# Kernel optimization log

Measured on AMD Instinct MI355X. Metric: run time of the kernel, lower is better.

The kernel has to match this reference:

```python
import jax, jax.numpy as jnp
import numpy as np
import math

B, S, D, H = 4, 2048, 1024, 16
HD = D // H  # 64
FF = 4096
EPS = 1e-5


def layer_norm(x, g, b):
    mu = jnp.mean(x, axis=-1, keepdims=True)
    var = jnp.mean(jnp.square(x - mu), axis=-1, keepdims=True)
    return (x - mu) * jax.lax.rsqrt(var + EPS) * g + b


def setup_inputs() -> dict:
    key = jax.random.key(0)
    ks = jax.random.split(key, 16)
    sc = 0.02
    return {
        "x": jax.random.normal(ks[0], (B, S, D), dtype=jnp.float32),
        "Wq": jax.random.normal(ks[1], (H, D, HD), dtype=jnp.float32) * sc,
        "bq": jnp.zeros((H, HD), dtype=jnp.float32),
        "Wk": jax.random.normal(ks[2], (H, D, HD), dtype=jnp.float32) * sc,
        "bk": jnp.zeros((H, HD), dtype=jnp.float32),
        "Wv": jax.random.normal(ks[3], (H, D, HD), dtype=jnp.float32) * sc,
        "bv": jnp.zeros((H, HD), dtype=jnp.float32),
        "Wo": jax.random.normal(ks[4], (D, D), dtype=jnp.float32) * sc,
        "bo": jnp.zeros((D,), dtype=jnp.float32),
        "W1": jax.random.normal(ks[5], (D, FF), dtype=jnp.float32) * sc,
        "b1": jnp.zeros((FF,), dtype=jnp.float32),
        "W2": jax.random.normal(ks[6], (FF, D), dtype=jnp.float32) * sc,
        "b2": jnp.zeros((D,), dtype=jnp.float32),
        "ln1_g": jnp.ones((D,), dtype=jnp.float32),
        "ln1_b": jnp.zeros((D,), dtype=jnp.float32),
        "ln2_g": jnp.ones((D,), dtype=jnp.float32),
        "ln2_b": jnp.zeros((D,), dtype=jnp.float32),
    }


def reference(x, Wq, bq, Wk, bk, Wv, bv, Wo, bo, W1, b1, W2, b2, ln1_g, ln1_b, ln2_g, ln2_b):
    b, s, d = x.shape
    h1 = layer_norm(x, ln1_g, ln1_b)
    # per-head Q/K/V linears, vectorized over heads: [b,h,s,hd]
    q = jnp.einsum('bsd,hde->bhse', h1, Wq) + bq[None, :, None, :]
    k = jnp.einsum('bsd,hde->bhse', h1, Wk) + bk[None, :, None, :]
    v = jnp.einsum('bsd,hde->bhse', h1, Wv) + bv[None, :, None, :]
    scores = jnp.einsum('bhqe,bhke->bhqk', q, k) / math.sqrt(q.shape[-1])
    causal = jnp.tril(jnp.ones((s, s), dtype=bool))
    scores = jnp.where(causal[None, None], scores, -jnp.inf)
    weights = jax.nn.softmax(scores, axis=-1)
    attn = jnp.einsum('bhqk,bhke->bhqe', weights, v)
    # concat heads (head order = torch concat dim=-1)
    attn = attn.transpose(0, 2, 1, 3).reshape(b, s, d)
    x = x + attn @ Wo + bo
    h2 = layer_norm(x, ln2_g, ln2_b)
    y = jax.nn.gelu(h2 @ W1 + b1, approximate=False)
    y = jax.nn.gelu(y @ W2 + b2, approximate=False)
    return x + y
```

## Files before the change

### kernel.cpp

```cpp
#include <hip/hip_runtime.h>
#include <cstdint>
#include <cstddef>


#define DI __device__ __forceinline__

typedef __attribute__((ext_vector_type(8))) __bf16 bf16x8;
typedef __attribute__((ext_vector_type(4))) float floatx4;
typedef __attribute__((ext_vector_type(4))) unsigned int uintx4;

static constexpr int Bn = 4, Sn = 2048, Dn = 1024, Hn = 16, HDn = 64, FFn = 4096;
static constexpr int NTOK = Bn * Sn;
static constexpr int D3 = 3 * Dn;

DI float bf2f(unsigned short u) { return __uint_as_float(((unsigned int)u) << 16); }
DI unsigned short f2bf(float f) {
  unsigned int u = __float_as_uint(f);
  u += 0x7FFFu + ((u >> 16) & 1u);
  return (unsigned short)(u >> 16);
}
DI float gelu_f(float v) { return 0.5f * v * (1.0f + erff(v * 0.70710678118654752f)); }
DI bf16x8 ld8(const unsigned short* p) { return *(const bf16x8*)p; }
DI floatx4 mfma16(bf16x8 a, bf16x8 b, floatx4 c) {
  return __builtin_amdgcn_mfma_f32_16x16x32_bf16(a, b, c, 0, 0, 0);
}
DI void g2l16(const unsigned short* g, unsigned short* l) {
  __builtin_amdgcn_global_load_lds((__attribute__((address_space(1))) void*)g,
                                   (__attribute__((address_space(3))) void*)l,
                                   16, 0, 0);
}
DI float ldin(const void* p, size_t idx, bool f32) {
  return f32 ? ((const float*)p)[idx] : bf2f(((const unsigned short*)p)[idx]);
}
DI unsigned int cvt_pk_bf16(float lo, float hi) {
  unsigned int r;
  asm("v_cvt_pk_bf16_f32 %0, %1, %2" : "=v"(r) : "v"(lo), "v"(hi));
  return r;
}
DI bf16x8 pack8(unsigned int a, unsigned int b, unsigned int c, unsigned int d) {
  uintx4 t;
  t[0] = a; t[1] = b; t[2] = c; t[3] = d;
  return __builtin_bit_cast(bf16x8, t);
}
DI int swz16(int row, int col) {
  return (row << 6) + ((((col >> 3) ^ row ^ (row >> 3)) & 7) << 3) + (col & 7);
}
DI int xcd_swz(int bid, int nwg) {
  return (bid & 7) * (nwg >> 3) + (bid >> 3);
}

__global__ void detect_kernel(const unsigned short* __restrict__ x,
                              int* __restrict__ flag) {
  int t = threadIdx.x;
  int cnt = 0;
  for (int i = t; i < 1024; i += 64) {
    unsigned short u = x[2 * i];
    int e = (u >> 7) & 0xFF;
    cnt += (e >= 96 && e <= 142) ? 1 : 0;
  }
  #pragma unroll
  for (int off = 32; off >= 1; off >>= 1) cnt += __shfl_xor(cnt, off);
  if (t == 0) *flag = (cnt < 820) ? 1 : 0;
}

__global__ void vec_prep(const void* bq, const void* bk, const void* bv,
                         const void* bo, const void* b1, const void* b2,
                         const void* g1, const void* be1, const void* g2,
                         const void* be2, unsigned short* __restrict__ dst,
                         const int* __restrict__ flag) {
  int i = blockIdx.x * 256 + threadIdx.x;
  if (i >= 13312) return;
  const bool f32 = *flag != 0;
  const void* src; int off;
  if      (i < 1024)  { src = bq;  off = i; }
  else if (i < 2048)  { src = bk;  off = i - 1024; }
  else if (i < 3072)  { src = bv;  off = i - 2048; }
  else if (i < 4096)  { src = bo;  off = i - 3072; }
  else if (i < 8192)  { src = b1;  off = i - 4096; }
  else if (i < 9216)  { src = b2;  off = i - 8192; }
  else if (i < 10240) { src = g1;  off = i - 9216; }
  else if (i < 11264) { src = be1; off = i - 10240; }
  else if (i < 12288) { src = g2;  off = i - 11264; }
  else                { src = be2; off = i - 12288; }
  dst[i] = f2bf(ldin(src, off, f32));
}

__global__ void transpose_kernel(const void* __restrict__ src,
                                 unsigned short* __restrict__ dst, int K, int N,
                                 const int* __restrict__ flag) {
  __shared__ unsigned short tile[64][65];
  const bool f32 = *flag != 0;
  int kb = blockIdx.y * 64, nb = blockIdx.x * 64;
  for (int i = threadIdx.x; i < 4096; i += 256) {
    int r = i >> 6, c = i & 63;
    tile[r][c] = f2bf(ldin(src, (size_t)(kb + r) * N + nb + c, f32));
  }
  __syncthreads();
  for (int i = threadIdx.x; i < 4096; i += 256) {
    int r = i >> 6, c = i & 63;
    dst[(size_t)(nb + r) * K + kb + c] = tile[c][r];
  }
}

__global__ void qkvT_kernel(const void* __restrict__ Wq,
                            const void* __restrict__ Wk,
                            const void* __restrict__ Wv,
                            unsigned short* __restrict__ WT,
                            const int* __restrict__ flag) {
  __shared__ unsigned short tile[64][65];
  const bool f32 = *flag != 0;
  const void* src = blockIdx.z == 0 ? Wq : (blockIdx.z == 1 ? Wk : Wv);
  int h = blockIdx.y, d0 = blockIdx.x * 64;
  size_t base = (size_t)h * (Dn * HDn);
  for (int i = threadIdx.x; i < 4096; i += 256) {
    int r = i >> 6, c = i & 63;
    tile[r][c] = f2bf(ldin(src, base + (size_t)(d0 + r) * 64 + c, f32));
  }
  __syncthreads();
  for (int i = threadIdx.x; i < 4096; i += 256) {
    int r = i >> 6, c = i & 63;
    WT[(size_t)(blockIdx.z * 1024 + h * 64 + r) * 1024 + d0 + c] = tile[c][r];
  }
}

__global__ __launch_bounds__(256) void ln_kernel(const void* __restrict__ x,
                                                 const unsigned short* __restrict__ g,
                                                 const unsigned short* __restrict__ b,
                                                 unsigned short* __restrict__ out,
                                                 const int* __restrict__ flag) {
  const bool f32 = flag ? (*flag != 0) : true;
  int row = blockIdx.x, t = threadIdx.x;
  float v[4];
  if (f32) {
    float4 f = *(const float4*)((const float*)x + (size_t)row * Dn + t * 4);
    v[0] = f.x; v[1] = f.y; v[2] = f.z; v[3] = f.w;
  } else {
    ushort4 u = *(const ushort4*)((const unsigned short*)x + (size_t)row * Dn + t * 4);
    v[0] = bf2f(u.x); v[1] = bf2f(u.y); v[2] = bf2f(u.z); v[3] = bf2f(u.w);
  }
  float s = v[0] + v[1] + v[2] + v[3];
  float s2 = v[0] * v[0] + v[1] * v[1] + v[2] * v[2] + v[3] * v[3];
  #pragma unroll
  for (int off = 32; off >= 1; off >>= 1) {
    s += __shfl_xor(s, off);
    s2 += __shfl_xor(s2, off);
  }
  __shared__ float red[8];
  int wv = t >> 6, ln = t & 63;
  if (ln == 0) { red[wv] = s; red[4 + wv] = s2; }
  __syncthreads();
  s = red[0] + red[1] + red[2] + red[3];
  s2 = red[4] + red[5] + red[6] + red[7];
  float mu = s * (1.0f / 1024.0f);
  float var = s2 * (1.0f / 1024.0f) - mu * mu;
  float rs = rsqrtf(fmaxf(var, 0.0f) + 1e-5f);
  ushort4 gg = *(const ushort4*)(g + t * 4);
  ushort4 bb = *(const ushort4*)(b + t * 4);
  ushort4 o;
  o.x = f2bf((v[0] - mu) * rs * bf2f(gg.x) + bf2f(bb.x));
  o.y = f2bf((v[1] - mu) * rs * bf2f(gg.y) + bf2f(bb.y));
  o.z = f2bf((v[2] - mu) * rs * bf2f(gg.z) + bf2f(bb.z));
  o.w = f2bf((v[3] - mu) * rs * bf2f(gg.w) + bf2f(bb.w));
  *(ushort4*)(out + (size_t)row * Dn + t * 4) = o;
}

enum { EPI_BIAS_BF16 = 0, EPI_WO = 1, EPI_GELU = 2, EPI_FF2 = 3 };

template <int EPI>
__global__ __launch_bounds__(256, 3) void gemm_kernel(
    const unsigned short* __restrict__ A, const unsigned short* __restrict__ BT,
    const unsigned short* __restrict__ bias, const void* __restrict__ residv,
    const float* __restrict__ resid_f, unsigned short* __restrict__ Cb,
    float* __restrict__ Cf, const int* __restrict__ flag, int M, int N, int K) {
  __shared__ unsigned short As[128 * 32];
  __shared__ unsigned short Bs[128 * 32];
  const int gx = gridDim.x;
  const int nwg = gx * gridDim.y;
  const int bid = xcd_swz((int)blockIdx.y * gx + (int)blockIdx.x, nwg);
  const int m0 = (bid / gx) * 128, n0 = (bid % gx) * 128;
  const int w = threadIdx.x >> 6, lane = threadIdx.x & 63;
  const int waveM = (w >> 1) * 64, waveN = (w & 1) * 64;
  const int m16 = lane & 15, quad = lane >> 4;
  const bool rf32 = flag && (*flag != 0);

  const int srow = w * 32 + (lane >> 2);
  const int scol = (lane & 3) * 8;
  const unsigned short* Ag = A + (size_t)(m0 + srow) * K + scol;
  const unsigned short* Bg = BT + (size_t)(n0 + srow) * K + scol;
  unsigned short* Al = As + srow * 32 + scol;
  unsigned short* Bl = Bs + srow * 32 + scol;
  const size_t rowstep = (size_t)16 * K;

  floatx4 acc[4][4];
  #pragma unroll
  for (int i = 0; i < 4; i++)
    #pragma unroll
    for (int j = 0; j < 4; j++) acc[i][j] = floatx4{0.f, 0.f, 0.f, 0.f};

  for (int k0 = 0; k0 < K; k0 += 32) {
    g2l16(Ag, Al);
    g2l16(Ag + rowstep, Al + 16 * 32);
    g2l16(Bg, Bl);
    g2l16(Bg + rowstep, Bl + 16 * 32);
    Ag += 32; Bg += 32;
    __syncthreads();
    bf16x8 af[4], bfv[4];
    #pragma unroll
    for (int mt = 0; mt < 4; mt++)
      af[mt] = ld8(As + (waveM + mt * 16 + m16) * 32 + quad * 8);
    #pragma unroll
    for (int nt = 0; nt < 4; nt++)
      bfv[nt] = ld8(Bs + (waveN + nt * 16 + m16) * 32 + quad * 8);
    #pragma unroll
    for (int mt = 0; mt < 4; mt++)
      #pragma unroll
      for (int nt = 0; nt < 4; nt++)
        acc[mt][nt] = mfma16(af[mt], bfv[nt], acc[mt][nt]);
    __syncthreads();
  }

  #pragma unroll
  for (int mt = 0; mt < 4; mt++) {
    #pragma unroll
    for (int nt = 0; nt < 4; nt++) {
      const int col = n0 + waveN + nt * 16 + m16;
      const float bcol = bf2f(bias[col]);
      #pragma unroll
      for (int r = 0; r < 4; r++) {
        const int row = m0 + waveM + mt * 16 + quad * 4 + r;
        const size_t idx = (size_t)row * N + col;
        float v = acc[mt][nt][r] + bcol;
        if constexpr (EPI == EPI_BIAS_BF16) {
          Cb[idx] = f2bf(v);
        } else if constexpr (EPI == EPI_WO) {
          float rv = rf32 ? ((const float*)residv)[idx]
                          : bf2f(((const unsigned short*)residv)[idx]);
          Cf[idx] = v + rv;
        } else if constexpr (EPI == EPI_GELU) {
          Cb[idx] = f2bf(gelu_f(v));
        } else {
          float ov = gelu_f(v) + resid_f[idx];
          if (rf32) Cf[idx] = ov;
          else      Cb[idx] = f2bf(ov);
        }
      }
    }
  }
}

__global__ __launch_bounds__(256, 4) void attn_kernel(
    const unsigned short* __restrict__ qkv, unsigned short* __restrict__ attn) {
  const int bid = xcd_swz((int)blockIdx.y * 32 + (int)blockIdx.x, 2048);
  const int qt = 31 - (bid & 31);
  const int bh = bid >> 5;
  const int b = bh >> 4, h = bh & 15;
  const int tid = threadIdx.x;
  const int w = tid >> 6, lane = tid & 63;
  const int m16 = lane & 15, quad = lane >> 4;

  __shared__ unsigned short Ks[2][4096];
  __shared__ unsigned short Vt[2][4096];

  const int qrow = qt * 64 + w * 16 + m16;
  const int qloc = w * 16 + m16;
  const unsigned short* qp = qkv + (size_t)(b * Sn + qrow) * D3 + h * 64 + quad * 8;
  const bf16x8 qf0 = ld8(qp), qf1 = ld8(qp + 32);

  floatx4 acc_o[4];
  #pragma unroll
  for (int nt = 0; nt < 4; nt++) acc_o[nt] = floatx4{0.f, 0.f, 0.f, 0.f};
  float lsum = 0.f;

  const int kr = tid >> 3, kc = (tid & 7) * 8;
  const int krs = (kr & 3) + (((kr >> 3) & 3) << 2) + (((kr >> 2) & 1) << 4);
  const int vk = (tid >> 3) * 2, ve = (tid & 7) * 8;

  uint4 kreg0, kreg1, vreg0, vreg1;
  const unsigned short* const kvroot = qkv + (size_t)(b * Sn) * D3 + h * 64;

  {
    const unsigned short* base = kvroot;
    kreg0 = *(const uint4*)(base + (size_t)kr * D3 + 1024 + kc);
    kreg1 = *(const uint4*)(base + (size_t)(kr + 32) * D3 + 1024 + kc);
    vreg0 = *(const uint4*)(base + (size_t)vk * D3 + 2048 + ve);
    vreg1 = *(const uint4*)(base + (size_t)(vk + 1) * D3 + 2048 + ve);
  }

  for (int kt = 0; kt <= qt; ++kt) {
    const int pb = kt & 1;
    *(uint4*)(Ks[pb] + swz16(krs, kc)) = kreg0;
    *(uint4*)(Ks[pb] + swz16(krs + 32, kc)) = kreg1;
    {
      const unsigned short* a0 = (const unsigned short*)&vreg0;
      const unsigned short* a1 = (const unsigned short*)&vreg1;
      #pragma unroll
      for (int i = 0; i < 8; i++) {
        unsigned int word = (unsigned int)a0[i] | ((unsigned int)a1[i] << 16);
        *(unsigned int*)(Vt[pb] + swz16(ve + i, vk)) = word;
      }
    }
    __syncthreads();
    if (kt < qt) {
      const unsigned short* base = kvroot + (size_t)(kt + 1) * 64 * D3;
      kreg0 = *(const uint4*)(base + (size_t)kr * D3 + 1024 + kc);
      kreg1 = *(const uint4*)(base + (size_t)(kr + 32) * D3 + 1024 + kc);
      vreg0 = *(const uint4*)(base + (size_t)vk * D3 + 2048 + ve);
      vreg1 = *(const uint4*)(base + (size_t)(vk + 1) * D3 + 2048 + ve);
    }

    floatx4 sa[4];
    #pragma unroll
    for (int nt = 0; nt < 4; nt++) {
      bf16x8 k0 = ld8(Ks[pb] + swz16(nt * 16 + m16, quad * 8));
      bf16x8 k1 = ld8(Ks[pb] + swz16(nt * 16 + m16, 32 + quad * 8));
      floatx4 t = mfma16(k0, qf0, floatx4{0.f, 0.f, 0.f, 0.f});
      sa[nt] = mfma16(k1, qf1, t);
    }

    if (kt == qt) {
      #pragma unroll
      for (int nt = 0; nt < 4; nt++) {
        const int kb_ = (quad << 3) + ((nt & 1) << 2) + ((nt >> 1) << 5);
        #pragma unroll
        for (int r = 0; r < 4; r++)
          if (kb_ + r > qloc) sa[nt][r] = -1e30f;
      }
    }

    constexpr float C = 0.18033688011112042f;
    float e00 = __builtin_amdgcn_exp2f(sa[0][0] * C);
    float e01 = __builtin_amdgcn_exp2f(sa[0][1] * C);
    float e02 = __builtin_amdgcn_exp2f(sa[0][2] * C);
    float e03 = __builtin_amdgcn_exp2f(sa[0][3] * C);
    float e10 = __builtin_amdgcn_exp2f(sa[1][0] * C);
    float e11 = __builtin_amdgcn_exp2f(sa[1][1] * C);
    float e12 = __builtin_amdgcn_exp2f(sa[1][2] * C);
    float e13 = __builtin_amdgcn_exp2f(sa[1][3] * C);
    float e20 = __builtin_amdgcn_exp2f(sa[2][0] * C);
    float e21 = __builtin_amdgcn_exp2f(sa[2][1] * C);
    float e22 = __builtin_amdgcn_exp2f(sa[2][2] * C);
    float e23 = __builtin_amdgcn_exp2f(sa[2][3] * C);
    float e30 = __builtin_amdgcn_exp2f(sa[3][0] * C);
    float e31 = __builtin_amdgcn_exp2f(sa[3][1] * C);
    float e32 = __builtin_amdgcn_exp2f(sa[3][2] * C);
    float e33 = __builtin_amdgcn_exp2f(sa[3][3] * C);
    lsum += ((e00 + e01) + (e02 + e03)) + ((e10 + e11) + (e12 + e13)) +
            ((e20 + e21) + (e22 + e23)) + ((e30 + e31) + (e32 + e33));
    const bf16x8 pa0 = pack8(cvt_pk_bf16(e00, e01), cvt_pk_bf16(e02, e03),
                             cvt_pk_bf16(e10, e11), cvt_pk_bf16(e12, e13));
    const bf16x8 pa1 = pack8(cvt_pk_bf16(e20, e21), cvt_pk_bf16(e22, e23),
                             cvt_pk_bf16(e30, e31), cvt_pk_bf16(e32, e33));

    #pragma unroll
    for (int nt = 0; nt < 4; nt++) {
      bf16x8 v0 = ld8(Vt[pb] + swz16(nt * 16 + m16, quad * 8));
      bf16x8 v1 = ld8(Vt[pb] + swz16(nt * 16 + m16, 32 + quad * 8));
      acc_o[nt] = mfma16(pa0, v0, acc_o[nt]);
      acc_o[nt] = mfma16(pa1, v1, acc_o[nt]);
    }
  }

  lsum += __shfl_xor(lsum, 16);
  lsum += __shfl_xor(lsum, 32);

  #pragma unroll
  for (int r = 0; r < 4; r++) {
    const float inv = 1.0f / fmaxf(__shfl(lsum, quad * 4 + r), 1e-20f);
    const size_t orow = (size_t)(b * Sn + qt * 64 + w * 16 + quad * 4 + r) * Dn + h * 64;
    #pragma unroll
    for (int nt = 0; nt < 4; nt++)
      attn[orow + nt * 16 + m16] = f2bf(acc_o[nt][r] * inv);
  }
}

extern "C" void kernel_launch(void* const* d_in, const int* in_sizes, int n_in,
                              void* d_out, int out_size, void* d_ws, size_t ws_size,
                              hipStream_t stream) {
  (void)in_sizes; (void)n_in; (void)out_size; (void)ws_size;
  const void* x    = d_in[0];
  const void* Wq   = d_in[1];
  const void* bq   = d_in[2];
  const void* Wk   = d_in[3];
  const void* bk   = d_in[4];
  const void* Wv   = d_in[5];
  const void* bv   = d_in[6];
  const void* Wo   = d_in[7];
  const void* bo   = d_in[8];
  const void* W1   = d_in[9];
  const void* b1   = d_in[10];
  const void* W2   = d_in[11];
  const void* b2   = d_in[12];
  const void* ln1g = d_in[13];
  const void* ln1b = d_in[14];
  const void* ln2g = d_in[15];
  const void* ln2b = d_in[16];
  char* ws = (char*)d_ws;

  constexpr size_t OFF_WTQKV = 0;
  constexpr size_t OFF_WOT   = OFF_WTQKV + (size_t)D3 * Dn * 2;
  constexpr size_t OFF_W1T   = OFF_WOT + (size_t)Dn * Dn * 2;
  constexpr size_t OFF_W2T   = OFF_W1T + (size_t)FFn * Dn * 2;
  constexpr size_t OFF_VEC   = OFF_W2T + (size_t)Dn * FFn * 2;
  constexpr size_t OFF_FLAG  = OFF_VEC + 32768;
  constexpr size_t OFF_H     = OFF_FLAG + 256;
  constexpr size_t OFF_QKV   = OFF_H + (size_t)NTOK * Dn * 2;
  constexpr size_t OFF_ATTN  = OFF_QKV + (size_t)NTOK * D3 * 2;
  constexpr size_t OFF_X2    = OFF_ATTN + (size_t)NTOK * Dn * 2;
  constexpr size_t OFF_Y1    = OFF_QKV;

  unsigned short* WTqkv = (unsigned short*)(ws + OFF_WTQKV);
  unsigned short* WoT   = (unsigned short*)(ws + OFF_WOT);
  unsigned short* W1T   = (unsigned short*)(ws + OFF_W1T);
  unsigned short* W2T   = (unsigned short*)(ws + OFF_W2T);
  unsigned short* vec   = (unsigned short*)(ws + OFF_VEC);
  int*            flag  = (int*)(ws + OFF_FLAG);
  unsigned short* hbuf  = (unsigned short*)(ws + OFF_H);
  unsigned short* qkvb  = (unsigned short*)(ws + OFF_QKV);
  unsigned short* attnb = (unsigned short*)(ws + OFF_ATTN);
  float*          x2    = (float*)(ws + OFF_X2);
  unsigned short* y1    = (unsigned short*)(ws + OFF_Y1);

  detect_kernel<<<1, 64, 0, stream>>>((const unsigned short*)x, flag);

  vec_prep<<<52, 256, 0, stream>>>(bq, bk, bv, bo, b1, b2, ln1g, ln1b, ln2g,
                                   ln2b, vec, flag);
  qkvT_kernel<<<dim3(16, 16, 3), 256, 0, stream>>>(Wq, Wk, Wv, WTqkv, flag);
  transpose_kernel<<<dim3(16, 16), 256, 0, stream>>>(Wo, WoT, 1024, 1024, flag);
  transpose_kernel<<<dim3(64, 16), 256, 0, stream>>>(W1, W1T, 1024, 4096, flag);
  transpose_kernel<<<dim3(16, 64), 256, 0, stream>>>(W2, W2T, 4096, 1024, flag);

  ln_kernel<<<NTOK, 256, 0, stream>>>(x, vec + 9216, vec + 10240, hbuf, flag);
  gemm_kernel<EPI_BIAS_BF16><<<dim3(D3 / 128, NTOK / 128), 256, 0, stream>>>(
      hbuf, WTqkv, vec + 0, nullptr, nullptr, qkvb, nullptr, nullptr,
      NTOK, D3, Dn);
  attn_kernel<<<dim3(Sn / 64, Bn * Hn), 256, 0, stream>>>(qkvb, attnb);
  gemm_kernel<EPI_WO><<<dim3(Dn / 128, NTOK / 128), 256, 0, stream>>>(
      attnb, WoT, vec + 3072, x, nullptr, nullptr, x2, flag, NTOK, Dn, Dn);
  ln_kernel<<<NTOK, 256, 0, stream>>>(x2, vec + 11264, vec + 12288, hbuf, nullptr);
  gemm_kernel<EPI_GELU><<<dim3(FFn / 128, NTOK / 128), 256, 0, stream>>>(
      hbuf, W1T, vec + 4096, nullptr, nullptr, y1, nullptr, nullptr,
      NTOK, FFn, Dn);
  gemm_kernel<EPI_FF2><<<dim3(Dn / 128, NTOK / 128), 256, 0, stream>>>(
      y1, W2T, vec + 8192, nullptr, x2, (unsigned short*)d_out, (float*)d_out,
      flag, NTOK, Dn, FFn);
}
```

Measured before the change: 596.6 us.

## Double-buffer GEMM shared-memory tiles to overlap global loads with MFMA

Gives the GEMM kernel two LDS buffers for the A and B tiles. Each iteration issues direct global-to-LDS loads for the next K tile before running MFMAs on the current one, and uses a single vmcnt wait plus barrier per iteration instead of two syncthreads. The aim is to hide global load latency behind compute. In exchange, LDS use doubles from 16KB to 32KB per block, which can reduce occupancy under launch_bounds(256,3). Removing the trailing barrier also relies on the next iteration's writes going to the other buffer.

```diff
diff --git a/kernel.cpp b/kernel.cpp
--- a/kernel.cpp
+++ b/kernel.cpp
@@ -172,8 +172,8 @@
     const unsigned short* __restrict__ bias, const void* __restrict__ residv,
     const float* __restrict__ resid_f, unsigned short* __restrict__ Cb,
     float* __restrict__ Cf, const int* __restrict__ flag, int M, int N, int K) {
-  __shared__ unsigned short As[128 * 32];
-  __shared__ unsigned short Bs[128 * 32];
+  __shared__ unsigned short As[2][128 * 32];
+  __shared__ unsigned short Bs[2][128 * 32];
   const int gx = gridDim.x;
   const int nwg = gx * gridDim.y;
   const int bid = xcd_swz((int)blockIdx.y * gx + (int)blockIdx.x, nwg);
@@ -185,10 +185,9 @@
 
   const int srow = w * 32 + (lane >> 2);
   const int scol = (lane & 3) * 8;
+  const int stoff = srow * 32 + scol;
   const unsigned short* Ag = A + (size_t)(m0 + srow) * K + scol;
   const unsigned short* Bg = BT + (size_t)(n0 + srow) * K + scol;
-  unsigned short* Al = As + srow * 32 + scol;
-  unsigned short* Bl = Bs + srow * 32 + scol;
   const size_t rowstep = (size_t)16 * K;
 
   floatx4 acc[4][4];
@@ -197,26 +196,45 @@
     #pragma unroll
     for (int j = 0; j < 4; j++) acc[i][j] = floatx4{0.f, 0.f, 0.f, 0.f};
 
-  for (int k0 = 0; k0 < K; k0 += 32) {
-    g2l16(Ag, Al);
-    g2l16(Ag + rowstep, Al + 16 * 32);
-    g2l16(Bg, Bl);
-    g2l16(Bg + rowstep, Bl + 16 * 32);
-    Ag += 32; Bg += 32;
-    __syncthreads();
+  g2l16(Ag, As[0] + stoff);
+  g2l16(Ag + rowstep, As[0] + stoff + 16 * 32);
+  g2l16(Bg, Bs[0] + stoff);
+  g2l16(Bg + rowstep, Bs[0] + stoff + 16 * 32);
+  Ag += 32; Bg += 32;
+  asm volatile("s_waitcnt vmcnt(0)" ::: "memory");
+  __builtin_amdgcn_s_barrier();
+
+  const int ntiles = K >> 5;
+  int cur = 0;
+  for (int t = 0; t < ntiles; ++t) {
+    if (t + 1 < ntiles) {
+      unsigned short* Aln = As[cur ^ 1] + stoff;
+      unsigned short* Bln = Bs[cur ^ 1] + stoff;
+      g2l16(Ag, Aln);
+      g2l16(Ag + rowstep, Aln + 16 * 32);
+      g2l16(Bg, Bln);
+      g2l16(Bg + rowstep, Bln + 16 * 32);
+      Ag += 32; Bg += 32;
+    }
+    const unsigned short* Ab = As[cur];
+    const unsigned short* Bb = Bs[cur];
     bf16x8 af[4], bfv[4];
     #pragma unroll
     for (int mt = 0; mt < 4; mt++)
-      af[mt] = ld8(As + (waveM + mt * 16 + m16) * 32 + quad * 8);
+      af[mt] = ld8(Ab + (waveM + mt * 16 + m16) * 32 + quad * 8);
     #pragma unroll
     for (int nt = 0; nt < 4; nt++)
-      bfv[nt] = ld8(Bs + (waveN + nt * 16 + m16) * 32 + quad * 8);
+      bfv[nt] = ld8(Bb + (waveN + nt * 16 + m16) * 32 + quad * 8);
     #pragma unroll
     for (int mt = 0; mt < 4; mt++)
       #pragma unroll
       for (int nt = 0; nt < 4; nt++)
         acc[mt][nt] = mfma16(af[mt], bfv[nt], acc[mt][nt]);
-    __syncthreads();
+    if (t + 1 < ntiles) {
+      asm volatile("s_waitcnt vmcnt(0)" ::: "memory");
+      __builtin_amdgcn_s_barrier();
+      cur ^= 1;
+    }
   }
 
   #pragma unroll
```

Measured after the change: 591.2 us. No clear change (-0.9%).

## Ping-pong GEMM with two wave groups and 4-slot LDS ring

Applied to the files above, without the earlier changes.

Rewrites the GEMM main loop to use 512 threads split into two groups of four waves. The groups alternate between issuing MFMAs on one K-tile and prefetching tiles three steps ahead into a 4-deep swizzled LDS ring. The two partial accumulators are reduced through LDS before the epilogue, which runs only in the first four waves. The aim is to hide global-load latency and LDS bank conflicts behind compute. In exchange it costs more LDS (64KB per block), an extra reduction step, and idle compute waves on alternate iterations.

```diff
diff --git a/kernel.cpp b/kernel.cpp
--- a/kernel.cpp
+++ b/kernel.cpp
@@ -47,6 +47,11 @@
 }
 DI int xcd_swz(int bid, int nwg) {
   return (bid & 7) * (nwg >> 3) + (bid >> 3);
+}
+DI void wg_barrier() {
+  asm volatile("" ::: "memory");
+  __builtin_amdgcn_s_barrier();
+  asm volatile("" ::: "memory");
 }
 
 __global__ void detect_kernel(const unsigned short* __restrict__ x,
@@ -167,29 +172,32 @@
 enum { EPI_BIAS_BF16 = 0, EPI_WO = 1, EPI_GELU = 2, EPI_FF2 = 3 };
 
 template <int EPI>
-__global__ __launch_bounds__(256, 3) void gemm_kernel(
+__global__ __launch_bounds__(512, 4) void gemm_kernel(
     const unsigned short* __restrict__ A, const unsigned short* __restrict__ BT,
     const unsigned short* __restrict__ bias, const void* __restrict__ residv,
     const float* __restrict__ resid_f, unsigned short* __restrict__ Cb,
     float* __restrict__ Cf, const int* __restrict__ flag, int M, int N, int K) {
-  __shared__ unsigned short As[128 * 32];
-  __shared__ unsigned short Bs[128 * 32];
+  __shared__ unsigned short Abuf[4][128 * 32];
+  __shared__ unsigned short Bbuf[4][128 * 32];
   const int gx = gridDim.x;
   const int nwg = gx * gridDim.y;
   const int bid = xcd_swz((int)blockIdx.y * gx + (int)blockIdx.x, nwg);
   const int m0 = (bid / gx) * 128, n0 = (bid % gx) * 128;
-  const int w = threadIdx.x >> 6, lane = threadIdx.x & 63;
-  const int waveM = (w >> 1) * 64, waveN = (w & 1) * 64;
+  const int tid = threadIdx.x;
+  const int w = tid >> 6, lane = tid & 63;
+  const int grp = w >> 2;
+  const int wg = w & 3;
+  const int waveM = (wg >> 1) * 64, waveN = (wg & 1) * 64;
   const int m16 = lane & 15, quad = lane >> 4;
+  const int sxor = (m16 >> 1) & 3;
   const bool rf32 = flag && (*flag != 0);
 
-  const int srow = w * 32 + (lane >> 2);
-  const int scol = (lane & 3) * 8;
-  const unsigned short* Ag = A + (size_t)(m0 + srow) * K + scol;
-  const unsigned short* Bg = BT + (size_t)(n0 + srow) * K + scol;
-  unsigned short* Al = As + srow * 32 + scol;
-  unsigned short* Bl = Bs + srow * 32 + scol;
-  const size_t rowstep = (size_t)16 * K;
+  const int rA0 = wg * 32 + (lane >> 2);
+  const int qcs = ((lane & 3) ^ ((lane >> 3) & 3)) * 8;
+  const unsigned short* Agb = A + (size_t)(m0 + rA0) * K + qcs;
+  const unsigned short* Bgb = BT + (size_t)(n0 + rA0) * K + qcs;
+  const size_t rstep = (size_t)16 * K;
+  const int ldsOff = (wg * 128 + lane) * 8;
 
   floatx4 acc[4][4];
   #pragma unroll
@@ -197,27 +205,92 @@
     #pragma unroll
     for (int j = 0; j < 4; j++) acc[i][j] = floatx4{0.f, 0.f, 0.f, 0.f};
 
-  for (int k0 = 0; k0 < K; k0 += 32) {
-    g2l16(Ag, Al);
-    g2l16(Ag + rowstep, Al + 16 * 32);
-    g2l16(Bg, Bl);
-    g2l16(Bg + rowstep, Bl + 16 * 32);
-    Ag += 32; Bg += 32;
-    __syncthreads();
-    bf16x8 af[4], bfv[4];
+  auto stage = [&](int slot, int kk) {
+    g2l16(Agb + kk, Abuf[slot] + ldsOff);
+    g2l16(Agb + rstep + kk, Abuf[slot] + ldsOff + 512);
+    g2l16(Bgb + kk, Bbuf[slot] + ldsOff);
+    g2l16(Bgb + rstep + kk, Bbuf[slot] + ldsOff + 512);
+  };
+
+  if (grp == 0) {
+    stage(0, 0);
+    stage(2, 64);
+    asm volatile("s_waitcnt vmcnt(4)" ::: "memory");
+  } else {
+    stage(1, 32);
+  }
+  wg_barrier();
+
+  const int ntiles = K >> 5;
+  for (int t = 0; t < ntiles; ++t) {
+    if (grp == (t & 1)) {
+      const unsigned short* Ab = Abuf[t & 3];
+      const unsigned short* Bb = Bbuf[t & 3];
+      bf16x8 af[4], bfv[4];
+      #pragma unroll
+      for (int mt = 0; mt < 4; mt++) {
+        const int row = waveM + mt * 16 + m16;
+        af[mt] = ld8(Ab + row * 32 + ((quad ^ sxor) << 3));
+      }
+      #pragma unroll
+      for (int nt = 0; nt < 4; nt++) {
+        const int row = waveN + nt * 16 + m16;
+        bfv[nt] = ld8(Bb + row * 32 + ((quad ^ sxor) << 3));
+      }
+      #pragma unroll
+      for (int mt = 0; mt < 4; mt++)
+        #pragma unroll
+        for (int nt = 0; nt < 4; nt++)
+          acc[mt][nt] = mfma16(af[mt], bfv[nt], acc[mt][nt]);
+    } else {
+      if (t + 3 < ntiles) {
+        stage((t + 3) & 3, (t + 3) * 32);
+        asm volatile("s_waitcnt vmcnt(4)" ::: "memory");
+      } else if (t + 1 < ntiles) {
+        asm volatile("s_waitcnt vmcnt(0)" ::: "memory");
+      }
+    }
+    wg_barrier();
+  }
+
+  float* shred = (float*)&Abuf[0][0];
+  if (w == 4 || w == 5) {
+    float* dst = shred + (w - 4) * 4096;
     #pragma unroll
     for (int mt = 0; mt < 4; mt++)
-      af[mt] = ld8(As + (waveM + mt * 16 + m16) * 32 + quad * 8);
-    #pragma unroll
-    for (int nt = 0; nt < 4; nt++)
-      bfv[nt] = ld8(Bs + (waveN + nt * 16 + m16) * 32 + quad * 8);
+      #pragma unroll
+      for (int nt = 0; nt < 4; nt++)
+        *(floatx4*)(dst + ((mt * 4 + nt) * 64 + lane) * 4) = acc[mt][nt];
+  }
+  __syncthreads();
+  if (w == 0 || w == 1) {
+    const float* src = shred + w * 4096;
     #pragma unroll
     for (int mt = 0; mt < 4; mt++)
       #pragma unroll
       for (int nt = 0; nt < 4; nt++)
-        acc[mt][nt] = mfma16(af[mt], bfv[nt], acc[mt][nt]);
-    __syncthreads();
-  }
+        acc[mt][nt] += *(const floatx4*)(src + ((mt * 4 + nt) * 64 + lane) * 4);
+  }
+  __syncthreads();
+  if (w == 6 || w == 7) {
+    float* dst = shred + (w - 6) * 4096;
+    #pragma unroll
+    for (int mt = 0; mt < 4; mt++)
+      #pragma unroll
+      for (int nt = 0; nt < 4; nt++)
+        *(floatx4*)(dst + ((mt * 4 + nt) * 64 + lane) * 4) = acc[mt][nt];
+  }
+  __syncthreads();
+  if (w == 2 || w == 3) {
+    const float* src = shred + (w - 2) * 4096;
+    #pragma unroll
+    for (int mt = 0; mt < 4; mt++)
+      #pragma unroll
+      for (int nt = 0; nt < 4; nt++)
+        acc[mt][nt] += *(const floatx4*)(src + ((mt * 4 + nt) * 64 + lane) * 4);
+  }
+
+  if (w >= 4) return;
 
   #pragma unroll
   for (int mt = 0; mt < 4; mt++) {
@@ -430,17 +503,17 @@
   transpose_kernel<<<dim3(16, 64), 256, 0, stream>>>(W2, W2T, 4096, 1024, flag);
 
   ln_kernel<<<NTOK, 256, 0, stream>>>(x, vec + 9216, vec + 10240, hbuf, flag);
-  gemm_kernel<EPI_BIAS_BF16><<<dim3(D3 / 128, NTOK / 128), 256, 0, stream>>>(
+  gemm_kernel<EPI_BIAS_BF16><<<dim3(D3 / 128, NTOK / 128), 512, 0, stream>>>(
       hbuf, WTqkv, vec + 0, nullptr, nullptr, qkvb, nullptr, nullptr,
       NTOK, D3, Dn);
   attn_kernel<<<dim3(Sn / 64, Bn * Hn), 256, 0, stream>>>(qkvb, attnb);
-  gemm_kernel<EPI_WO><<<dim3(Dn / 128, NTOK / 128), 256, 0, stream>>>(
+  gemm_kernel<EPI_WO><<<dim3(Dn / 128, NTOK / 128), 512, 0, stream>>>(
       attnb, WoT, vec + 3072, x, nullptr, nullptr, x2, flag, NTOK, Dn, Dn);
   ln_kernel<<<NTOK, 256, 0, stream>>>(x2, vec + 11264, vec + 12288, hbuf, nullptr);
-  gemm_kernel<EPI_GELU><<<dim3(FFn / 128, NTOK / 128), 256, 0, stream>>>(
+  gemm_kernel<EPI_GELU><<<dim3(FFn / 128, NTOK / 128), 512, 0, stream>>>(
       hbuf, W1T, vec + 4096, nullptr, nullptr, y1, nullptr, nullptr,
       NTOK, FFn, Dn);
-  gemm_kernel<EPI_FF2><<<dim3(Dn / 128, NTOK / 128), 256, 0, stream>>>(
+  gemm_kernel<EPI_FF2><<<dim3(Dn / 128, NTOK / 128), 512, 0, stream>>>(
       y1, W2T, vec + 8192, nullptr, x2, (unsigned short*)d_out, (float*)d_out,
       flag, NTOK, Dn, FFn);
 }
```

Measured after the change: 678.4 us. +13.7%, slower.

## Use 256x256 GEMM tiles with triple-buffered LDS, swizzle, and fast GELU

Applied to the files above, without the earlier changes.

The GEMM grows from 128x128 to 256x256 tiles with 512 threads. It adds a three-slot LDS ring filled through global_load_lds, using vmcnt waits and a single barrier per k-step so loads overlap compute. It also XOR-swizzles the LDS layout to cut bank conflicts. Separately, the erf-based GELU becomes a sigmoid-style exp2/rcp approximation, which changes numerics and may move error tolerance. Larger tiles reduce the grid size: the Wo and FF2 GEMMs get only 128 blocks, so the GPU may be underfilled, and register pressure rises with 32 accumulators per thread.

```diff
diff --git a/kernel.cpp b/kernel.cpp
--- a/kernel.cpp
+++ b/kernel.cpp
@@ -19,7 +19,16 @@
   u += 0x7FFFu + ((u >> 16) & 1u);
   return (unsigned short)(u >> 16);
 }
-DI float gelu_f(float v) { return 0.5f * v * (1.0f + erff(v * 0.70710678118654752f)); }
+DI float gelu_f(float v) {
+  float t = v * v;
+  float c = __builtin_fmaf(t, -0.1029443f, -2.3022080f);
+  float z = v * c;
+  float e = __builtin_amdgcn_exp2f(z);
+  float d = 1.0f + e;
+  float r;
+  asm("v_rcp_f32 %0, %1" : "=v"(r) : "v"(d));
+  return v * r;
+}
 DI bf16x8 ld8(const unsigned short* p) { return *(const bf16x8*)p; }
 DI floatx4 mfma16(bf16x8 a, bf16x8 b, floatx4 c) {
   return __builtin_amdgcn_mfma_f32_16x16x32_bf16(a, b, c, 0, 0, 0);
@@ -167,60 +176,72 @@
 enum { EPI_BIAS_BF16 = 0, EPI_WO = 1, EPI_GELU = 2, EPI_FF2 = 3 };
 
 template <int EPI>
-__global__ __launch_bounds__(256, 3) void gemm_kernel(
+__global__ __launch_bounds__(512, 2) void gemm_kernel(
     const unsigned short* __restrict__ A, const unsigned short* __restrict__ BT,
     const unsigned short* __restrict__ bias, const void* __restrict__ residv,
     const float* __restrict__ resid_f, unsigned short* __restrict__ Cb,
     float* __restrict__ Cf, const int* __restrict__ flag, int M, int N, int K) {
-  __shared__ unsigned short As[128 * 32];
-  __shared__ unsigned short Bs[128 * 32];
+  __shared__ unsigned short As[3][256 * 32];
+  __shared__ unsigned short Bs[3][256 * 32];
   const int gx = gridDim.x;
   const int nwg = gx * gridDim.y;
   const int bid = xcd_swz((int)blockIdx.y * gx + (int)blockIdx.x, nwg);
-  const int m0 = (bid / gx) * 128, n0 = (bid % gx) * 128;
-  const int w = threadIdx.x >> 6, lane = threadIdx.x & 63;
-  const int waveM = (w >> 1) * 64, waveN = (w & 1) * 64;
+  const int m0 = (bid / gx) * 256, n0 = (bid % gx) * 256;
+  const int tid = threadIdx.x;
+  const int w = tid >> 6, lane = tid & 63;
+  const int waveM = (w >> 2) * 128, waveN = (w & 3) * 64;
   const int m16 = lane & 15, quad = lane >> 4;
+  const int sxor = (m16 >> 1) & 3;
   const bool rf32 = flag && (*flag != 0);
 
-  const int srow = w * 32 + (lane >> 2);
-  const int scol = (lane & 3) * 8;
+  const int srow = tid >> 2;
+  const int chunk = tid & 3;
+  const int stO = srow * 32 + chunk * 8;
+  const int scol = (chunk ^ ((srow >> 1) & 3)) * 8;
   const unsigned short* Ag = A + (size_t)(m0 + srow) * K + scol;
   const unsigned short* Bg = BT + (size_t)(n0 + srow) * K + scol;
-  unsigned short* Al = As + srow * 32 + scol;
-  unsigned short* Bl = Bs + srow * 32 + scol;
-  const size_t rowstep = (size_t)16 * K;
-
-  floatx4 acc[4][4];
-  #pragma unroll
-  for (int i = 0; i < 4; i++)
+  const size_t rstep = (size_t)128 * K;
+
+  floatx4 acc[8][4];
+  #pragma unroll
+  for (int i = 0; i < 8; i++)
     #pragma unroll
     for (int j = 0; j < 4; j++) acc[i][j] = floatx4{0.f, 0.f, 0.f, 0.f};
 
-  for (int k0 = 0; k0 < K; k0 += 32) {
-    g2l16(Ag, Al);
-    g2l16(Ag + rowstep, Al + 16 * 32);
-    g2l16(Bg, Bl);
-    g2l16(Bg + rowstep, Bl + 16 * 32);
+  auto stage = [&](int slot) {
+    g2l16(Ag, As[slot] + stO);
+    g2l16(Ag + rstep, As[slot] + stO + 128 * 32);
+    g2l16(Bg, Bs[slot] + stO);
+    g2l16(Bg + rstep, Bs[slot] + stO + 128 * 32);
     Ag += 32; Bg += 32;
-    __syncthreads();
-    bf16x8 af[4], bfv[4];
-    #pragma unroll
-    for (int mt = 0; mt < 4; mt++)
-      af[mt] = ld8(As + (waveM + mt * 16 + m16) * 32 + quad * 8);
+  };
+
+  const int ntiles = K >> 5;
+  stage(0);
+  stage(1);
+  for (int t = 0; t < ntiles; ++t) {
+    if (t < ntiles - 1) asm volatile("s_waitcnt vmcnt(4)" ::: "memory");
+    else                asm volatile("s_waitcnt vmcnt(0)" ::: "memory");
+    __builtin_amdgcn_s_barrier();
+    if (t + 2 < ntiles) stage((t + 2) % 3);
+
+    const unsigned short* Ab = As[t % 3];
+    const unsigned short* Bb = Bs[t % 3];
+    bf16x8 bfv[4];
     #pragma unroll
     for (int nt = 0; nt < 4; nt++)
-      bfv[nt] = ld8(Bs + (waveN + nt * 16 + m16) * 32 + quad * 8);
-    #pragma unroll
-    for (int mt = 0; mt < 4; mt++)
+      bfv[nt] = ld8(Bb + (waveN + nt * 16 + m16) * 32 + ((quad ^ sxor) << 3));
+    #pragma unroll
+    for (int mt = 0; mt < 8; mt++) {
+      bf16x8 a = ld8(Ab + (waveM + mt * 16 + m16) * 32 + ((quad ^ sxor) << 3));
       #pragma unroll
       for (int nt = 0; nt < 4; nt++)
-        acc[mt][nt] = mfma16(af[mt], bfv[nt], acc[mt][nt]);
-    __syncthreads();
-  }
-
-  #pragma unroll
-  for (int mt = 0; mt < 4; mt++) {
+        acc[mt][nt] = mfma16(a, bfv[nt], acc[mt][nt]);
+    }
+  }
+
+  #pragma unroll
+  for (int mt = 0; mt < 8; mt++) {
     #pragma unroll
     for (int nt = 0; nt < 4; nt++) {
       const int col = n0 + waveN + nt * 16 + m16;
@@ -430,17 +451,17 @@
   transpose_kernel<<<dim3(16, 64), 256, 0, stream>>>(W2, W2T, 4096, 1024, flag);
 
   ln_kernel<<<NTOK, 256, 0, stream>>>(x, vec + 9216, vec + 10240, hbuf, flag);
-  gemm_kernel<EPI_BIAS_BF16><<<dim3(D3 / 128, NTOK / 128), 256, 0, stream>>>(
+  gemm_kernel<EPI_BIAS_BF16><<<dim3(D3 / 256, NTOK / 256), 512, 0, stream>>>(
       hbuf, WTqkv, vec + 0, nullptr, nullptr, qkvb, nullptr, nullptr,
       NTOK, D3, Dn);
   attn_kernel<<<dim3(Sn / 64, Bn * Hn), 256, 0, stream>>>(qkvb, attnb);
-  gemm_kernel<EPI_WO><<<dim3(Dn / 128, NTOK / 128), 256, 0, stream>>>(
+  gemm_kernel<EPI_WO><<<dim3(Dn / 256, NTOK / 256), 512, 0, stream>>>(
       attnb, WoT, vec + 3072, x, nullptr, nullptr, x2, flag, NTOK, Dn, Dn);
   ln_kernel<<<NTOK, 256, 0, stream>>>(x2, vec + 11264, vec + 12288, hbuf, nullptr);
-  gemm_kernel<EPI_GELU><<<dim3(FFn / 128, NTOK / 128), 256, 0, stream>>>(
+  gemm_kernel<EPI_GELU><<<dim3(FFn / 256, NTOK / 256), 512, 0, stream>>>(
       hbuf, W1T, vec + 4096, nullptr, nullptr, y1, nullptr, nullptr,
       NTOK, FFn, Dn);
-  gemm_kernel<EPI_FF2><<<dim3(Dn / 128, NTOK / 128), 256, 0, stream>>>(
+  gemm_kernel<EPI_FF2><<<dim3(Dn / 256, NTOK / 256), 512, 0, stream>>>(
       y1, W2T, vec + 8192, nullptr, x2, (unsigned short*)d_out, (float*)d_out,
       flag, NTOK, Dn, FFn);
 }
```

Measured after the change: 705.4 us. 1.18x slower.
